# Kernel optimization log

Measured on AMD Instinct MI355X. Metric: run time of the kernel, lower is better.

## Reference

```python
import jax, jax.numpy as jnp
import numpy as np

N_NODES = 50000
N_EDGES = 1600000
IN_DIM = 128
HEADS = 4
OUT_DIM = 32
LEAKY_SLOPE = 0.2
BETA = 0.5
C = 1.2


def setup_inputs() -> dict:
    key = jax.random.key(0)
    k1, k2, k3, k4, k5, k6 = jax.random.split(key, 6)
    x = jax.random.normal(k1, (N_NODES, IN_DIM), dtype=jnp.float32)
    edge_index = jax.random.randint(k2, (2, N_EDGES), 0, N_NODES, dtype=jnp.int64)
    # GATConv params: shared linear (no bias), per-head attention vectors, output bias
    glorot = 1.0 / np.sqrt(IN_DIM)
    W = jax.random.uniform(k3, (IN_DIM, HEADS * OUT_DIM), jnp.float32, -glorot, glorot)
    att_src = jax.random.uniform(k4, (HEADS, OUT_DIM), jnp.float32, -glorot, glorot)
    att_dst = jax.random.uniform(k5, (HEADS, OUT_DIM), jnp.float32, -glorot, glorot)
    bias = jnp.zeros((HEADS * OUT_DIM,), jnp.float32)
    return {"x": x, "edge_index": edge_index, "W": W,
            "att_src": att_src, "att_dst": att_dst, "bias": bias}


def reference(x, edge_index, W, att_src, att_dst, bias):
    N = x.shape[0]
    H, D = att_src.shape
    # add self loops (edge j->i aggregates at i)
    loop = jnp.arange(N, dtype=edge_index.dtype)
    src = jnp.concatenate([edge_index[0], loop])  # [Etot]
    dst = jnp.concatenate([edge_index[1], loop])
    # per-head projection
    xp = (x @ W).reshape(N, H, D)                 # [N,H,D]
    a_src = jnp.einsum('nhd,hd->nh', xp, att_src)  # [N,H]
    a_dst = jnp.einsum('nhd,hd->nh', xp, att_dst)
    alpha = jax.nn.leaky_relu(a_src[src] + a_dst[dst], LEAKY_SLOPE)  # [Etot,H]
    # scatter-softmax over incoming edges per target node (self loops ensure coverage)
    amax = jax.ops.segment_max(alpha, dst, num_segments=N)
    e = jnp.exp(alpha - amax[dst])
    denom = jax.ops.segment_sum(e, dst, num_segments=N)
    w = e / (denom[dst] + 1e-16)                  # [Etot,H]
    # weighted scatter-add aggregation
    msg = xp[src] * w[:, :, None]                 # [Etot,H,D]
    out = jax.ops.segment_sum(msg, dst, num_segments=N).reshape(N, H * D)
    z = out + bias
    # beta-mix Swish (non-learnable swish beta = 1)
    return BETA * z + (C - BETA) * (z * jax.nn.sigmoid(z))
```

## Files before the change

### kernel.cpp

```cpp
#include <hip/hip_runtime.h>
#include <hip/hip_bf16.h>
#include <hip/hip_fp16.h>
#include <stdint.h>

#define LEAKY 0.2f
#define MIX_BETA 0.5f
#define MIX_C 1.2f

#define FBITS 6
#define FSZ   (1 << FBITS)
#define NBMX  1024
#define CH    3072
#define EPT   12
#define CAPP  2944

using short8 = __attribute__((ext_vector_type(8))) short;
using f32x4  = __attribute__((ext_vector_type(4))) float;

__device__ __forceinline__ unsigned f2bf(float f) {
    unsigned u = __float_as_uint(f);
    return (u + 0x7fffu + ((u >> 16) & 1u)) >> 16;
}
__device__ __forceinline__ unsigned pack2bf(float a, float b) {
    return f2bf(a) | (f2bf(b) << 16);
}
__device__ __forceinline__ float hlo(unsigned u) {
    return __half2float(__ushort_as_half((uint16_t)(u & 0xFFFFu)));
}
__device__ __forceinline__ float hhi(unsigned u) {
    return __half2float(__ushort_as_half((uint16_t)(u >> 16)));
}
__device__ __forceinline__ float leaky_exp(float v) {
    v = fmaxf(v, LEAKY * v);
    return __expf(v);
}

__global__ __launch_bounds__(512) void k_prep(const void* x, const void* ei, const void* W,
                                              const void* att_s, const void* att_d,
                                              const void* bias, int N, int* flags,
                                              float* att_sf, float* att_df, float* biasf,
                                              uint16_t* Wtg, int* gbcursor) {
    __shared__ uint16_t wt[128][136];
    __shared__ int lf[2];
    const int t = threadIdx.x;
    gbcursor[t] = 0; gbcursor[t + 512] = 0;
    if (t < 64) {
        const uint16_t* u = (const uint16_t*)x;
        uint16_t v = u[2 * t];
        int ef = (v >> 7) & 0xFF;
        bool ok = (ef >= 90 && ef <= 140);
        unsigned long long all_ok = __ballot(ok);
        const unsigned long long* e64 = (const unsigned long long*)ei;
        bool big = (e64[t] >= (unsigned long long)N);
        unsigned long long anybig = __ballot(big);
        if (t == 0) {
            int f0 = (all_ok == ~0ull) ? 1 : 0;
            int f1 = (anybig != 0ull) ? 1 : 0;
            flags[0] = f0; flags[1] = f1;
            lf[0] = f0; lf[1] = f1;
        }
    }
    __syncthreads();
    const bool bf = lf[0] != 0;
    if (t >= 64 && t < 448) {
        int i = t - 64;
        const void* in; float* out; int idx;
        if (i < 128)      { in = att_s; out = att_sf; idx = i; }
        else if (i < 256) { in = att_d; out = att_df; idx = i - 128; }
        else              { in = bias;  out = biasf;  idx = i - 256; }
        float v = bf ? __uint_as_float(((unsigned)((const uint16_t*)in)[idx]) << 16)
                     : ((const float*)in)[idx];
        out[idx] = v;
    }
    for (int s = t; s < 4096; s += 512) {
        int k = s >> 5, c4 = (s & 31) * 4;
        ushort4 hv;
        if (bf) {
            hv = *(const ushort4*)((const uint16_t*)W + k * 128 + c4);
        } else {
            float4 v = *(const float4*)((const float*)W + k * 128 + c4);
            hv.x = (uint16_t)f2bf(v.x); hv.y = (uint16_t)f2bf(v.y);
            hv.z = (uint16_t)f2bf(v.z); hv.w = (uint16_t)f2bf(v.w);
        }
        wt[c4 + 0][k] = hv.x; wt[c4 + 1][k] = hv.y;
        wt[c4 + 2][k] = hv.z; wt[c4 + 3][k] = hv.w;
    }
    __syncthreads();
    for (int s = t; s < 2048; s += 512) {
        int r = s >> 4, ch = (s & 15) * 8;
        *(int4*)(Wtg + r * 128 + ch) = *(const int4*)&wt[r][ch];
    }
}

__global__ __launch_bounds__(256) void k_mid(const void* x, const void* ei,
                                             const uint16_t* Wtg,
                                             const float* att_sf, const float* att_df,
                                             const int* flags, int N, int E, int G,
                                             int nb, int cap, int* gbcursor,
                                             unsigned* entries,
                                             unsigned* xph, float* a_src, float* a_dst) {
    __shared__ char smem[35840] __attribute__((aligned(16)));
    const int t = threadIdx.x;

    if ((int)blockIdx.x < G) {
        uint16_t (*xs)[136] = (uint16_t(*)[136])smem;
        const bool bf = flags[0] != 0;
        const int row0 = blockIdx.x * 128;

        for (int s = t; s < 4096; s += 256) {
            int r = s >> 5, kc = (s & 31) * 4;
            int rr = row0 + r; if (rr >= N) rr = N - 1;
            size_t g = (size_t)rr * 128 + kc;
            ushort4 hv;
            if (bf) {
                hv = *(const ushort4*)((const uint16_t*)x + g);
            } else {
                float4 v = *(const float4*)((const float*)x + g);
                hv.x = (uint16_t)f2bf(v.x); hv.y = (uint16_t)f2bf(v.y);
                hv.z = (uint16_t)f2bf(v.z); hv.w = (uint16_t)f2bf(v.w);
            }
            *(ushort4*)&xs[r][kc] = hv;
        }
        __syncthreads();

        const int w = t >> 6, l = t & 63;
        const int rA = l & 15;
        const int kg = (l >> 4) * 8;
        f32x4 acc[2][8];
#pragma unroll
        for (int fr = 0; fr < 2; ++fr)
#pragma unroll
            for (int fc = 0; fc < 8; ++fc) acc[fr][fc] = (f32x4){0.f, 0.f, 0.f, 0.f};

#pragma unroll
        for (int kk = 0; kk < 4; ++kk) {
            const int kb = kk * 32 + kg;
            short8 a0 = *(const short8*)&xs[w * 32 + rA][kb];
            short8 a1 = *(const short8*)&xs[w * 32 + 16 + rA][kb];
            const uint16_t* wp = Wtg + rA * 128 + kb;
#pragma unroll
            for (int fc = 0; fc < 8; ++fc) {
                short8 b = *(const short8*)(wp + fc * 2048);
                acc[0][fc] = __builtin_amdgcn_mfma_f32_16x16x32_bf16(a0, b, acc[0][fc], 0, 0, 0);
                acc[1][fc] = __builtin_amdgcn_mfma_f32_16x16x32_bf16(a1, b, acc[1][fc], 0, 0, 0);
            }
        }
        __syncthreads();

#pragma unroll
        for (int fr = 0; fr < 2; ++fr)
#pragma unroll
            for (int fc = 0; fc < 8; ++fc) {
                int row = w * 32 + fr * 16 + (l >> 4) * 4;
                int col = fc * 16 + rA;
#pragma unroll
                for (int j = 0; j < 4; ++j)
                    xs[row + j][col] = __half_as_ushort(__float2half(acc[fr][fc][j]));
            }
        __syncthreads();

        for (int s = t; s < 2048; s += 256) {
            int r = s >> 4, ch = (s & 15) * 8;
            int rr = row0 + r;
            if (rr < N)
                *(int4*)((uint16_t*)xph + (size_t)rr * 128 + ch) = *(const int4*)&xs[r][ch];
        }
        for (int s = t; s < 512; s += 256) {
            int r = s >> 2, hh = s & 3;
            int rr = row0 + r;
            if (rr < N) {
                float ss = 0.f, sd = 0.f;
#pragma unroll
                for (int q = 0; q < 32; ++q) {
                    float v = __half2float(__ushort_as_half(xs[r][hh * 32 + q]));
                    ss = fmaf(v, att_sf[hh * 32 + q], ss);
                    sd = fmaf(v, att_df[hh * 32 + q], sd);
                }
                a_src[(size_t)rr * 4 + hh] = ss;
                a_dst[(size_t)rr * 4 + hh] = sd;
            }
        }
    } else {
        unsigned* st  = (unsigned*)smem;
        uint16_t* bb  = (uint16_t*)(smem + 12288);
        int* lcnt     = (int*)(smem + 18432);
        int* loff     = (int*)(smem + 22528);
        int* lbase    = (int*)(smem + 26624);
        int* wcur     = (int*)(smem + 30720);
        int* sc       = (int*)(smem + 34816);
        const bool is32 = flags[1] != 0;
        const int chunk0 = ((int)blockIdx.x - G) * CH;
        const int nvalid = min(CH, E - chunk0);

        int se[EPT], de[EPT];
#pragma unroll
        for (int q = 0; q < 4; ++q) { lcnt[t + 256 * q] = 0; wcur[t + 256 * q] = 0; }
        __syncthreads();
#pragma unroll
        for (int k = 0; k < EPT; ++k) {
            int i = chunk0 + k * 256 + t;
            if (i < E) {
                int s, d;
                if (is32) { const int* p = (const int*)ei; s = p[i]; d = p[E + i]; }
                else { const long long* p = (const long long*)ei; s = (int)p[i]; d = (int)p[E + i]; }
                se[k] = s; de[k] = d;
                atomicAdd(&lcnt[d >> FBITS], 1);
            } else {
                de[k] = -1;
            }
        }
        __syncthreads();
        int c0 = lcnt[4 * t], c1 = lcnt[4 * t + 1], c2 = lcnt[4 * t + 2], c3 = lcnt[4 * t + 3];
        sc[t] = c0 + c1 + c2 + c3;
        __syncthreads();
        for (int o = 1; o < 256; o <<= 1) {
            int v = (t >= o) ? sc[t - o] : 0;
            __syncthreads();
            sc[t] += v;
            __syncthreads();
        }
        {
            int base0 = sc[t] - (c0 + c1 + c2 + c3);
            int off4[4] = {base0, base0 + c0, base0 + c0 + c1, base0 + c0 + c1 + c2};
            int cnt4[4] = {c0, c1, c2, c3};
#pragma unroll
            for (int q = 0; q < 4; ++q) {
                int k = 4 * t + q;
                loff[k] = off4[q];
                if (k < nb && cnt4[q]) {
                    int m = min(cnt4[q], cap);
                    int base = atomicAdd(&gbcursor[k], cnt4[q]);
                    if (base > cap - m) base = cap - m;
                    if (base < 0) base = 0;
                    lbase[k] = base;
                }
            }
        }
        __syncthreads();
#pragma unroll
        for (int k = 0; k < EPT; ++k) {
            int d = de[k];
            if (d >= 0) {
                int b = d >> FBITS;
                int slot = atomicAdd(&wcur[b], 1);
                int pos = loff[b] + slot;
                st[pos] = (unsigned)se[k] | ((unsigned)(d & (FSZ - 1)) << 17);
                bb[pos] = (uint16_t)b;
            }
        }
        __syncthreads();
        for (int s = t; s < nvalid; s += 256) {
            int b = bb[s];
            int pos = lbase[b] + (s - loff[b]);
            if (pos >= 0 && pos < cap)
                entries[(size_t)b * cap + pos] = st[s];
        }
    }
}

__global__ __launch_bounds__(512) void k_final(const unsigned* entries, const int* gbcursor,
                                               int cap, int N,
                                               const float* a_src, const float* a_dst,
                                               const unsigned* xph, const float* biasf,
                                               const int* flags, void* out) {
    __shared__ uint16_t ssrc_l[CAPP];
    __shared__ __half   ews_l[(CAPP / 4) * 16];
    __shared__ int ncnt[FSZ], nscan[FSZ], wcur[FSZ], poff[FSZ];
    __shared__ float adst_l[FSZ][4];
    const int b = blockIdx.x;
    const int t = threadIdx.x;
    const int node0 = b << FBITS;
    const size_t eb = (size_t)b * cap;
    const int count = min(gbcursor[b], cap);

    if (t < FSZ * 4) {
        int ln = t >> 2, hh = t & 3;
        int n = node0 + ln;
        adst_l[ln][hh] = (n < N) ? a_dst[(size_t)n * 4 + hh] : 0.f;
    }
    if (t < FSZ) ncnt[t] = 0;
    __syncthreads();
    unsigned er[6];
    int nr = 0;
    for (int i = t; i < count; i += 512) {
        unsigned e = entries[eb + i];
        er[nr++] = e;
        atomicAdd(&ncnt[e >> 17], 1);
    }
    __syncthreads();
    if (t < FSZ) nscan[t] = (ncnt[t] + 3) & ~3;
    __syncthreads();
    for (int o = 1; o < FSZ; o <<= 1) {
        int v = (t < FSZ && t >= o) ? nscan[t - o] : 0;
        __syncthreads();
        if (t < FSZ) nscan[t] += v;
        __syncthreads();
    }
    if (t < FSZ) {
        int pcnt = (ncnt[t] + 3) & ~3;
        int px = nscan[t] - pcnt;
        wcur[t] = px;
        poff[t] = px;
    }
    __syncthreads();
    if (t < FSZ) {
        int c = ncnt[t];
        int pcnt = (c + 3) & ~3;
        int px = poff[t];
        for (int p = c; p < pcnt; ++p) {
            int slot = px + p;
            ssrc_l[slot] = 0;
            __half* pe = &ews_l[(slot >> 2) * 16];
            int j = slot & 3;
            const __half z = __float2half(0.f);
            pe[j] = z; pe[4 + j] = z; pe[8 + j] = z; pe[12 + j] = z;
        }
    }
    for (int r = 0; r < nr; ++r) {
        unsigned e = er[r];
        int dlo = (int)(e >> 17);
        int s = (int)(e & 0x1FFFFu);
        int slot = atomicAdd(&wcur[dlo], 1);
        if (slot < CAPP) {
            float4 as = *(const float4*)(a_src + (size_t)s * 4);
            const float* ad = adst_l[dlo];
            float e0 = leaky_exp(as.x + ad[0]);
            float e1 = leaky_exp(as.y + ad[1]);
            float e2 = leaky_exp(as.z + ad[2]);
            float e3 = leaky_exp(as.w + ad[3]);
            ssrc_l[slot] = (uint16_t)s;
            __half* pe = &ews_l[(slot >> 2) * 16];
            int j = slot & 3;
            pe[j]      = __float2half(e0);
            pe[4 + j]  = __float2half(e1);
            pe[8 + j]  = __float2half(e2);
            pe[12 + j] = __float2half(e3);
        }
    }
    __syncthreads();

    const int wv = t >> 6, lane = t & 63;
    const int hi = lane >> 5;
    const int l = lane & 31;
    const int d0 = l * 4;
    const int h = l >> 3;
    const char* xb = (const char*)xph;
    const int outbf = flags[0];

    for (int k = wv; k < FSZ / 2; k += 8) {
        int ln = 2 * k + hi;
        int n = node0 + ln;
        bool ok = n < N;
        int nn = ok ? n : (N - 1);
        int nc = ok ? ncnt[ln] : 0;

        float adst = adst_l[ok ? ln : 0][h];
        float e = leaky_exp(a_src[(size_t)nn * 4 + h] + adst);
        uint2 xw = *(const uint2*)(xb + (size_t)nn * 256 + d0 * 2);
        float4 acc;
        acc.x = e * hlo(xw.x); acc.y = e * hhi(xw.x);
        acc.z = e * hlo(xw.y); acc.w = e * hhi(xw.y);
        float den = e;

        const int beg = ok ? poff[ln] : 0;
        const int gb = beg >> 2;
        const int ng = (nc + 3) >> 2;
        int g = 0;
        for (; g + 2 <= ng; g += 2) {
            ushort4 s4a = *(const ushort4*)&ssrc_l[beg + 4 * g];
            ushort4 s4b = *(const ushort4*)&ssrc_l[beg + 4 * g + 4];
            uint2 ea = *(const uint2*)&ews_l[(gb + g) * 16 + h * 4];
            uint2 ebw = *(const uint2*)&ews_l[(gb + g + 1) * 16 + h * 4];
            uint2 w0 = *(const uint2*)(xb + (size_t)s4a.x * 256 + d0 * 2);
            uint2 w1 = *(const uint2*)(xb + (size_t)s4a.y * 256 + d0 * 2);
            uint2 w2 = *(const uint2*)(xb + (size_t)s4a.z * 256 + d0 * 2);
            uint2 w3 = *(const uint2*)(xb + (size_t)s4a.w * 256 + d0 * 2);
            uint2 w4 = *(const uint2*)(xb + (size_t)s4b.x * 256 + d0 * 2);
            uint2 w5 = *(const uint2*)(xb + (size_t)s4b.y * 256 + d0 * 2);
            uint2 w6 = *(const uint2*)(xb + (size_t)s4b.z * 256 + d0 * 2);
            uint2 w7 = *(const uint2*)(xb + (size_t)s4b.w * 256 + d0 * 2);
            float e0 = hlo(ea.x), e1 = hhi(ea.x), e2 = hlo(ea.y), e3 = hhi(ea.y);
            float e4 = hlo(ebw.x), e5 = hhi(ebw.x), e6 = hlo(ebw.y), e7 = hhi(ebw.y);
            acc.x = fmaf(e0, hlo(w0.x), acc.x); acc.y = fmaf(e0, hhi(w0.x), acc.y);
            acc.z = fmaf(e0, hlo(w0.y), acc.z); acc.w = fmaf(e0, hhi(w0.y), acc.w);
            acc.x = fmaf(e1, hlo(w1.x), acc.x); acc.y = fmaf(e1, hhi(w1.x), acc.y);
            acc.z = fmaf(e1, hlo(w1.y), acc.z); acc.w = fmaf(e1, hhi(w1.y), acc.w);
            acc.x = fmaf(e2, hlo(w2.x), acc.x); acc.y = fmaf(e2, hhi(w2.x), acc.y);
            acc.z = fmaf(e2, hlo(w2.y), acc.z); acc.w = fmaf(e2, hhi(w2.y), acc.w);
            acc.x = fmaf(e3, hlo(w3.x), acc.x); acc.y = fmaf(e3, hhi(w3.x), acc.y);
            acc.z = fmaf(e3, hlo(w3.y), acc.z); acc.w = fmaf(e3, hhi(w3.y), acc.w);
            acc.x = fmaf(e4, hlo(w4.x), acc.x); acc.y = fmaf(e4, hhi(w4.x), acc.y);
            acc.z = fmaf(e4, hlo(w4.y), acc.z); acc.w = fmaf(e4, hhi(w4.y), acc.w);
            acc.x = fmaf(e5, hlo(w5.x), acc.x); acc.y = fmaf(e5, hhi(w5.x), acc.y);
            acc.z = fmaf(e5, hlo(w5.y), acc.z); acc.w = fmaf(e5, hhi(w5.y), acc.w);
            acc.x = fmaf(e6, hlo(w6.x), acc.x); acc.y = fmaf(e6, hhi(w6.x), acc.y);
            acc.z = fmaf(e6, hlo(w6.y), acc.z); acc.w = fmaf(e6, hhi(w6.y), acc.w);
            acc.x = fmaf(e7, hlo(w7.x), acc.x); acc.y = fmaf(e7, hhi(w7.x), acc.y);
            acc.z = fmaf(e7, hlo(w7.y), acc.z); acc.w = fmaf(e7, hhi(w7.y), acc.w);
            den += ((e0 + e1) + (e2 + e3)) + ((e4 + e5) + (e6 + e7));
        }
        if (g < ng) {
            ushort4 s4 = *(const ushort4*)&ssrc_l[beg + 4 * g];
            uint2 ea = *(const uint2*)&ews_l[(gb + g) * 16 + h * 4];
            float e0 = hlo(ea.x), e1 = hhi(ea.x), e2 = hlo(ea.y), e3 = hhi(ea.y);
            uint2 w0 = *(const uint2*)(xb + (size_t)s4.x * 256 + d0 * 2);
            uint2 w1 = *(const uint2*)(xb + (size_t)s4.y * 256 + d0 * 2);
            uint2 w2 = *(const uint2*)(xb + (size_t)s4.z * 256 + d0 * 2);
            uint2 w3 = *(const uint2*)(xb + (size_t)s4.w * 256 + d0 * 2);
            acc.x = fmaf(e0, hlo(w0.x), acc.x); acc.y = fmaf(e0, hhi(w0.x), acc.y);
            acc.z = fmaf(e0, hlo(w0.y), acc.z); acc.w = fmaf(e0, hhi(w0.y), acc.w);
            acc.x = fmaf(e1, hlo(w1.x), acc.x); acc.y = fmaf(e1, hhi(w1.x), acc.y);
            acc.z = fmaf(e1, hlo(w1.y), acc.z); acc.w = fmaf(e1, hhi(w1.y), acc.w);
            acc.x = fmaf(e2, hlo(w2.x), acc.x); acc.y = fmaf(e2, hhi(w2.x), acc.y);
            acc.z = fmaf(e2, hlo(w2.y), acc.z); acc.w = fmaf(e2, hhi(w2.y), acc.w);
            acc.x = fmaf(e3, hlo(w3.x), acc.x); acc.y = fmaf(e3, hhi(w3.x), acc.y);
            acc.z = fmaf(e3, hlo(w3.y), acc.z); acc.w = fmaf(e3, hhi(w3.y), acc.w);
            den += (e0 + e1) + (e2 + e3);
        }
        float inv = 1.f / (den + 1e-16f);
        float4 bv = *(const float4*)(biasf + d0);
        float z0 = fmaf(acc.x, inv, bv.x);
        float z1 = fmaf(acc.y, inv, bv.y);
        float z2 = fmaf(acc.z, inv, bv.z);
        float z3 = fmaf(acc.w, inv, bv.w);
        float r0 = MIX_BETA * z0 + (MIX_C - MIX_BETA) * z0 / (1.f + __expf(-z0));
        float r1 = MIX_BETA * z1 + (MIX_C - MIX_BETA) * z1 / (1.f + __expf(-z1));
        float r2 = MIX_BETA * z2 + (MIX_C - MIX_BETA) * z2 / (1.f + __expf(-z2));
        float r3 = MIX_BETA * z3 + (MIX_C - MIX_BETA) * z3 / (1.f + __expf(-z3));
        if (ok) {
            if (outbf) {
                uint2 ov = make_uint2(pack2bf(r0, r1), pack2bf(r2, r3));
                *(uint2*)((uint16_t*)out + (size_t)n * 128 + d0) = ov;
            } else {
                *(float4*)((float*)out + (size_t)n * 128 + d0) = make_float4(r0, r1, r2, r3);
            }
        }
    }
}

extern "C" void kernel_launch(void* const* d_in, const int* in_sizes, int n_in,
                              void* d_out, int out_size, void* d_ws, size_t ws_size,
                              hipStream_t stream) {
    const void* x     = d_in[0];
    const void* ei    = d_in[1];
    const void* W     = d_in[2];
    const void* att_s = d_in[3];
    const void* att_d = d_in[4];
    const void* bias  = d_in[5];
    const int N = in_sizes[0] / 128;
    const int E = in_sizes[1] / 2;
    const int NB = (N + FSZ - 1) >> FBITS;
    int cap = E / NB + E / (8 * NB) + 256;
    const int capmax = CAPP - 3 * FSZ - 8;
    if (cap > capmax) cap = capmax;

    char* ws = (char*)d_ws;
    size_t off = 0;
    auto alloc = [&](size_t bytes) -> void* {
        void* p = ws + off;
        off += (bytes + 255) & ~(size_t)255;
        return p;
    };
    int* flags        = (int*)alloc(16);
    unsigned* entries = (unsigned*)alloc((size_t)NB * cap * 4);
    int* gbcursor     = (int*)alloc(NBMX * 4);
    unsigned* xph     = (unsigned*)alloc((size_t)N * 64 * 4);
    float* a_src      = (float*)alloc((size_t)N * 4 * 4);
    float* a_dst      = (float*)alloc((size_t)N * 4 * 4);
    float* att_sf     = (float*)alloc(128 * 4);
    float* att_df     = (float*)alloc(128 * 4);
    float* biasf      = (float*)alloc(128 * 4);
    uint16_t* Wtg     = (uint16_t*)alloc(128 * 128 * 2);

    const int G = (N + 127) / 128;
    const int S = (E + CH - 1) / CH;

    k_prep<<<1, 512, 0, stream>>>(x, ei, W, att_s, att_d, bias, N, flags,
                                  att_sf, att_df, biasf, Wtg, gbcursor);
    k_mid<<<G + S, 256, 0, stream>>>(x, ei, Wtg, att_sf, att_df, flags, N, E, G,
                                     NB, cap, gbcursor, entries, xph, a_src, a_dst);
    k_final<<<NB, 512, 0, stream>>>(entries, gbcursor, cap, N, a_src, a_dst,
                                    xph, biasf, flags, d_out);
}
```

Measured before the change: 138.1 us.

## Double destination bucket size and widen per-lane gathers to 8 features

Destination buckets grow from 64 to 128 nodes, so there are fewer buckets, the binning chunks are larger and the final kernel runs with 1024 threads per block. In the aggregation loop each lane now loads 16-byte feature slices (8 halves) instead of 8 bytes, with 16 lanes covering a node and 4 nodes per wave. The goal is fewer, wider gather transactions and fewer global atomics on bucket cursors. The cost is much larger shared memory per final block and a larger capacity margin, which may lower occupancy and leave fewer blocks than CUs.

```diff
diff --git a/kernel.cpp b/kernel.cpp
--- a/kernel.cpp
+++ b/kernel.cpp
@@ -7,12 +7,12 @@
 #define MIX_BETA 0.5f
 #define MIX_C 1.2f
 
-#define FBITS 6
+#define FBITS 7
 #define FSZ   (1 << FBITS)
-#define NBMX  1024
-#define CH    3072
-#define EPT   12
-#define CAPP  2944
+#define NBMX  512
+#define CH    4096
+#define EPT   16
+#define CAPP  5632
 
 using short8 = __attribute__((ext_vector_type(8))) short;
 using f32x4  = __attribute__((ext_vector_type(4))) float;
@@ -33,6 +33,12 @@
 __device__ __forceinline__ float leaky_exp(float v) {
     v = fmaxf(v, LEAKY * v);
     return __expf(v);
+}
+__device__ __forceinline__ void fma8(float* acc, float e, uint4 w) {
+    acc[0] = fmaf(e, hlo(w.x), acc[0]); acc[1] = fmaf(e, hhi(w.x), acc[1]);
+    acc[2] = fmaf(e, hlo(w.y), acc[2]); acc[3] = fmaf(e, hhi(w.y), acc[3]);
+    acc[4] = fmaf(e, hlo(w.z), acc[4]); acc[5] = fmaf(e, hhi(w.z), acc[5]);
+    acc[6] = fmaf(e, hlo(w.w), acc[6]); acc[7] = fmaf(e, hhi(w.w), acc[7]);
 }
 
 __global__ __launch_bounds__(512) void k_prep(const void* x, const void* ei, const void* W,
@@ -43,7 +49,7 @@
     __shared__ uint16_t wt[128][136];
     __shared__ int lf[2];
     const int t = threadIdx.x;
-    gbcursor[t] = 0; gbcursor[t + 512] = 0;
+    if (t < NBMX) gbcursor[t] = 0;
     if (t < 64) {
         const uint16_t* u = (const uint16_t*)x;
         uint16_t v = u[2 * t];
@@ -99,7 +105,7 @@
                                              int nb, int cap, int* gbcursor,
                                              unsigned* entries,
                                              unsigned* xph, float* a_src, float* a_dst) {
-    __shared__ char smem[35840] __attribute__((aligned(16)));
+    __shared__ char smem[40960] __attribute__((aligned(16)));
     const int t = threadIdx.x;
 
     if ((int)blockIdx.x < G) {
@@ -182,19 +188,19 @@
         }
     } else {
         unsigned* st  = (unsigned*)smem;
-        uint16_t* bb  = (uint16_t*)(smem + 12288);
-        int* lcnt     = (int*)(smem + 18432);
-        int* loff     = (int*)(smem + 22528);
-        int* lbase    = (int*)(smem + 26624);
+        uint16_t* bb  = (uint16_t*)(smem + 16384);
+        int* lcnt     = (int*)(smem + 24576);
+        int* loff     = (int*)(smem + 26624);
+        int* lbase    = (int*)(smem + 28672);
         int* wcur     = (int*)(smem + 30720);
-        int* sc       = (int*)(smem + 34816);
+        int* sc       = (int*)(smem + 32768);
         const bool is32 = flags[1] != 0;
         const int chunk0 = ((int)blockIdx.x - G) * CH;
         const int nvalid = min(CH, E - chunk0);
 
         int se[EPT], de[EPT];
-#pragma unroll
-        for (int q = 0; q < 4; ++q) { lcnt[t + 256 * q] = 0; wcur[t + 256 * q] = 0; }
+        lcnt[t] = 0; lcnt[t + 256] = 0;
+        wcur[t] = 0; wcur[t + 256] = 0;
         __syncthreads();
 #pragma unroll
         for (int k = 0; k < EPT; ++k) {
@@ -210,8 +216,8 @@
             }
         }
         __syncthreads();
-        int c0 = lcnt[4 * t], c1 = lcnt[4 * t + 1], c2 = lcnt[4 * t + 2], c3 = lcnt[4 * t + 3];
-        sc[t] = c0 + c1 + c2 + c3;
+        int c0 = lcnt[2 * t], c1 = lcnt[2 * t + 1];
+        sc[t] = c0 + c1;
         __syncthreads();
         for (int o = 1; o < 256; o <<= 1) {
             int v = (t >= o) ? sc[t - o] : 0;
@@ -220,16 +226,17 @@
             __syncthreads();
         }
         {
-            int base0 = sc[t] - (c0 + c1 + c2 + c3);
-            int off4[4] = {base0, base0 + c0, base0 + c0 + c1, base0 + c0 + c1 + c2};
-            int cnt4[4] = {c0, c1, c2, c3};
-#pragma unroll
-            for (int q = 0; q < 4; ++q) {
-                int k = 4 * t + q;
-                loff[k] = off4[q];
-                if (k < nb && cnt4[q]) {
-                    int m = min(cnt4[q], cap);
-                    int base = atomicAdd(&gbcursor[k], cnt4[q]);
+            int excl = sc[t] - (c0 + c1);
+            int k0 = 2 * t, k1 = 2 * t + 1;
+            loff[k0] = excl;
+            loff[k1] = excl + c0;
+            int cnt2[2] = {c0, c1};
+#pragma unroll
+            for (int q = 0; q < 2; ++q) {
+                int k = k0 + q;
+                if (k < nb && cnt2[q]) {
+                    int m = min(cnt2[q], cap);
+                    int base = atomicAdd(&gbcursor[k], cnt2[q]);
                     if (base > cap - m) base = cap - m;
                     if (base < 0) base = 0;
                     lbase[k] = base;
@@ -258,11 +265,11 @@
     }
 }
 
-__global__ __launch_bounds__(512) void k_final(const unsigned* entries, const int* gbcursor,
-                                               int cap, int N,
-                                               const float* a_src, const float* a_dst,
-                                               const unsigned* xph, const float* biasf,
-                                               const int* flags, void* out) {
+__global__ __launch_bounds__(1024) void k_final(const unsigned* entries, const int* gbcursor,
+                                                int cap, int N,
+                                                const float* a_src, const float* a_dst,
+                                                const unsigned* xph, const float* biasf,
+                                                const int* flags, void* out) {
     __shared__ uint16_t ssrc_l[CAPP];
     __shared__ __half   ews_l[(CAPP / 4) * 16];
     __shared__ int ncnt[FSZ], nscan[FSZ], wcur[FSZ], poff[FSZ];
@@ -282,7 +289,7 @@
     __syncthreads();
     unsigned er[6];
     int nr = 0;
-    for (int i = t; i < count; i += 512) {
+    for (int i = t; i < count; i += 1024) {
         unsigned e = entries[eb + i];
         er[nr++] = e;
         atomicAdd(&ncnt[e >> 17], 1);
@@ -307,17 +314,17 @@
         int c = ncnt[t];
         int pcnt = (c + 3) & ~3;
         int px = poff[t];
+        const __half z = __float2half(0.f);
         for (int p = c; p < pcnt; ++p) {
             int slot = px + p;
             ssrc_l[slot] = 0;
             __half* pe = &ews_l[(slot >> 2) * 16];
             int j = slot & 3;
-            const __half z = __float2half(0.f);
             pe[j] = z; pe[4 + j] = z; pe[8 + j] = z; pe[12 + j] = z;
         }
     }
-    for (int r = 0; r < nr; ++r) {
-        unsigned e = er[r];
+    for (int r2 = 0; r2 < nr; ++r2) {
+        unsigned e = er[r2];
         int dlo = (int)(e >> 17);
         int s = (int)(e & 0x1FFFFu);
         int slot = atomicAdd(&wcur[dlo], 1);
@@ -340,15 +347,15 @@
     __syncthreads();
 
     const int wv = t >> 6, lane = t & 63;
-    const int hi = lane >> 5;
-    const int l = lane & 31;
-    const int d0 = l * 4;
-    const int h = l >> 3;
+    const int hi = lane >> 4;
+    const int l = lane & 15;
+    const int d0 = l * 8;
+    const int h = l >> 2;
     const char* xb = (const char*)xph;
     const int outbf = flags[0];
 
-    for (int k = wv; k < FSZ / 2; k += 8) {
-        int ln = 2 * k + hi;
+    for (int k = wv; k < FSZ / 4; k += 16) {
+        int ln = 4 * k + hi;
         int n = node0 + ln;
         bool ok = n < N;
         int nn = ok ? n : (N - 1);
@@ -356,10 +363,12 @@
 
         float adst = adst_l[ok ? ln : 0][h];
         float e = leaky_exp(a_src[(size_t)nn * 4 + h] + adst);
-        uint2 xw = *(const uint2*)(xb + (size_t)nn * 256 + d0 * 2);
-        float4 acc;
-        acc.x = e * hlo(xw.x); acc.y = e * hhi(xw.x);
-        acc.z = e * hlo(xw.y); acc.w = e * hhi(xw.y);
+        uint4 xw = *(const uint4*)(xb + (size_t)nn * 256 + d0 * 2);
+        float acc[8];
+        acc[0] = e * hlo(xw.x); acc[1] = e * hhi(xw.x);
+        acc[2] = e * hlo(xw.y); acc[3] = e * hhi(xw.y);
+        acc[4] = e * hlo(xw.z); acc[5] = e * hhi(xw.z);
+        acc[6] = e * hlo(xw.w); acc[7] = e * hhi(xw.w);
         float den = e;
 
         const int beg = ok ? poff[ln] : 0;
@@ -369,70 +378,58 @@
         for (; g + 2 <= ng; g += 2) {
             ushort4 s4a = *(const ushort4*)&ssrc_l[beg + 4 * g];
             ushort4 s4b = *(const ushort4*)&ssrc_l[beg + 4 * g + 4];
-            uint2 ea = *(const uint2*)&ews_l[(gb + g) * 16 + h * 4];
-            uint2 ebw = *(const uint2*)&ews_l[(gb + g + 1) * 16 + h * 4];
-            uint2 w0 = *(const uint2*)(xb + (size_t)s4a.x * 256 + d0 * 2);
-            uint2 w1 = *(const uint2*)(xb + (size_t)s4a.y * 256 + d0 * 2);
-            uint2 w2 = *(const uint2*)(xb + (size_t)s4a.z * 256 + d0 * 2);
-            uint2 w3 = *(const uint2*)(xb + (size_t)s4a.w * 256 + d0 * 2);
-            uint2 w4 = *(const uint2*)(xb + (size_t)s4b.x * 256 + d0 * 2);
-            uint2 w5 = *(const uint2*)(xb + (size_t)s4b.y * 256 + d0 * 2);
-            uint2 w6 = *(const uint2*)(xb + (size_t)s4b.z * 256 + d0 * 2);
-            uint2 w7 = *(const uint2*)(xb + (size_t)s4b.w * 256 + d0 * 2);
+            uint2 ea  = *(const uint2*)&ews_l[(gb + g) * 16 + h * 4];
+            uint2 eb2 = *(const uint2*)&ews_l[(gb + g + 1) * 16 + h * 4];
+            uint4 w0 = *(const uint4*)(xb + (size_t)s4a.x * 256 + d0 * 2);
+            uint4 w1 = *(const uint4*)(xb + (size_t)s4a.y * 256 + d0 * 2);
+            uint4 w2 = *(const uint4*)(xb + (size_t)s4a.z * 256 + d0 * 2);
+            uint4 w3 = *(const uint4*)(xb + (size_t)s4a.w * 256 + d0 * 2);
+            uint4 w4 = *(const uint4*)(xb + (size_t)s4b.x * 256 + d0 * 2);
+            uint4 w5 = *(const uint4*)(xb + (size_t)s4b.y * 256 + d0 * 2);
+            uint4 w6 = *(const uint4*)(xb + (size_t)s4b.z * 256 + d0 * 2);
+            uint4 w7 = *(const uint4*)(xb + (size_t)s4b.w * 256 + d0 * 2);
             float e0 = hlo(ea.x), e1 = hhi(ea.x), e2 = hlo(ea.y), e3 = hhi(ea.y);
-            float e4 = hlo(ebw.x), e5 = hhi(ebw.x), e6 = hlo(ebw.y), e7 = hhi(ebw.y);
-            acc.x = fmaf(e0, hlo(w0.x), acc.x); acc.y = fmaf(e0, hhi(w0.x), acc.y);
-            acc.z = fmaf(e0, hlo(w0.y), acc.z); acc.w = fmaf(e0, hhi(w0.y), acc.w);
-            acc.x = fmaf(e1, hlo(w1.x), acc.x); acc.y = fmaf(e1, hhi(w1.x), acc.y);
-            acc.z = fmaf(e1, hlo(w1.y), acc.z); acc.w = fmaf(e1, hhi(w1.y), acc.w);
-            acc.x = fmaf(e2, hlo(w2.x), acc.x); acc.y = fmaf(e2, hhi(w2.x), acc.y);
-            acc.z = fmaf(e2, hlo(w2.y), acc.z); acc.w = fmaf(e2, hhi(w2.y), acc.w);
-            acc.x = fmaf(e3, hlo(w3.x), acc.x); acc.y = fmaf(e3, hhi(w3.x), acc.y);
-            acc.z = fmaf(e3, hlo(w3.y), acc.z); acc.w = fmaf(e3, hhi(w3.y), acc.w);
-            acc.x = fmaf(e4, hlo(w4.x), acc.x); acc.y = fmaf(e4, hhi(w4.x), acc.y);
-            acc.z = fmaf(e4, hlo(w4.y), acc.z); acc.w = fmaf(e4, hhi(w4.y), acc.w);
-            acc.x = fmaf(e5, hlo(w5.x), acc.x); acc.y = fmaf(e5, hhi(w5.x), acc.y);
-            acc.z = fmaf(e5, hlo(w5.y), acc.z); acc.w = fmaf(e5, hhi(w5.y), acc.w);
-            acc.x = fmaf(e6, hlo(w6.x), acc.x); acc.y = fmaf(e6, hhi(w6.x), acc.y);
-            acc.z = fmaf(e6, hlo(w6.y), acc.z); acc.w = fmaf(e6, hhi(w6.y), acc.w);
-            acc.x = fmaf(e7, hlo(w7.x), acc.x); acc.y = fmaf(e7, hhi(w7.x), acc.y);
-            acc.z = fmaf(e7, hlo(w7.y), acc.z); acc.w = fmaf(e7, hhi(w7.y), acc.w);
+            float e4 = hlo(eb2.x), e5 = hhi(eb2.x), e6 = hlo(eb2.y), e7 = hhi(eb2.y);
+            fma8(acc, e0, w0); fma8(acc, e1, w1);
+            fma8(acc, e2, w2); fma8(acc, e3, w3);
+            fma8(acc, e4, w4); fma8(acc, e5, w5);
+            fma8(acc, e6, w6); fma8(acc, e7, w7);
             den += ((e0 + e1) + (e2 + e3)) + ((e4 + e5) + (e6 + e7));
         }
         if (g < ng) {
             ushort4 s4 = *(const ushort4*)&ssrc_l[beg + 4 * g];
             uint2 ea = *(const uint2*)&ews_l[(gb + g) * 16 + h * 4];
             float e0 = hlo(ea.x), e1 = hhi(ea.x), e2 = hlo(ea.y), e3 = hhi(ea.y);
-            uint2 w0 = *(const uint2*)(xb + (size_t)s4.x * 256 + d0 * 2);
-            uint2 w1 = *(const uint2*)(xb + (size_t)s4.y * 256 + d0 * 2);
-            uint2 w2 = *(const uint2*)(xb + (size_t)s4.z * 256 + d0 * 2);
-            uint2 w3 = *(const uint2*)(xb + (size_t)s4.w * 256 + d0 * 2);
-            acc.x = fmaf(e0, hlo(w0.x), acc.x); acc.y = fmaf(e0, hhi(w0.x), acc.y);
-            acc.z = fmaf(e0, hlo(w0.y), acc.z); acc.w = fmaf(e0, hhi(w0.y), acc.w);
-            acc.x = fmaf(e1, hlo(w1.x), acc.x); acc.y = fmaf(e1, hhi(w1.x), acc.y);
-            acc.z = fmaf(e1, hlo(w1.y), acc.z); acc.w = fmaf(e1, hhi(w1.y), acc.w);
-            acc.x = fmaf(e2, hlo(w2.x), acc.x); acc.y = fmaf(e2, hhi(w2.x), acc.y);
-            acc.z = fmaf(e2, hlo(w2.y), acc.z); acc.w = fmaf(e2, hhi(w2.y), acc.w);
-            acc.x = fmaf(e3, hlo(w3.x), acc.x); acc.y = fmaf(e3, hhi(w3.x), acc.y);
-            acc.z = fmaf(e3, hlo(w3.y), acc.z); acc.w = fmaf(e3, hhi(w3.y), acc.w);
+            uint4 w0 = *(const uint4*)(xb + (size_t)s4.x * 256 + d0 * 2);
+            uint4 w1 = *(const uint4*)(xb + (size_t)s4.y * 256 + d0 * 2);
+            uint4 w2 = *(const uint4*)(xb + (size_t)s4.z * 256 + d0 * 2);
+            uint4 w3 = *(const uint4*)(xb + (size_t)s4.w * 256 + d0 * 2);
+            fma8(acc, e0, w0); fma8(acc, e1, w1);
+            fma8(acc, e2, w2); fma8(acc, e3, w3);
             den += (e0 + e1) + (e2 + e3);
         }
         float inv = 1.f / (den + 1e-16f);
-        float4 bv = *(const float4*)(biasf + d0);
-        float z0 = fmaf(acc.x, inv, bv.x);
-        float z1 = fmaf(acc.y, inv, bv.y);
-        float z2 = fmaf(acc.z, inv, bv.z);
-        float z3 = fmaf(acc.w, inv, bv.w);
-        float r0 = MIX_BETA * z0 + (MIX_C - MIX_BETA) * z0 / (1.f + __expf(-z0));
-        float r1 = MIX_BETA * z1 + (MIX_C - MIX_BETA) * z1 / (1.f + __expf(-z1));
-        float r2 = MIX_BETA * z2 + (MIX_C - MIX_BETA) * z2 / (1.f + __expf(-z2));
-        float r3 = MIX_BETA * z3 + (MIX_C - MIX_BETA) * z3 / (1.f + __expf(-z3));
+        float4 bv0 = *(const float4*)(biasf + d0);
+        float4 bv1 = *(const float4*)(biasf + d0 + 4);
+        float z[8];
+        z[0] = fmaf(acc[0], inv, bv0.x); z[1] = fmaf(acc[1], inv, bv0.y);
+        z[2] = fmaf(acc[2], inv, bv0.z); z[3] = fmaf(acc[3], inv, bv0.w);
+        z[4] = fmaf(acc[4], inv, bv1.x); z[5] = fmaf(acc[5], inv, bv1.y);
+        z[6] = fmaf(acc[6], inv, bv1.z); z[7] = fmaf(acc[7], inv, bv1.w);
+        float r[8];
+#pragma unroll
+        for (int j = 0; j < 8; ++j)
+            r[j] = MIX_BETA * z[j] + (MIX_C - MIX_BETA) * z[j] / (1.f + __expf(-z[j]));
         if (ok) {
             if (outbf) {
-                uint2 ov = make_uint2(pack2bf(r0, r1), pack2bf(r2, r3));
-                *(uint2*)((uint16_t*)out + (size_t)n * 128 + d0) = ov;
+                uint4 ov;
+                ov.x = pack2bf(r[0], r[1]); ov.y = pack2bf(r[2], r[3]);
+                ov.z = pack2bf(r[4], r[5]); ov.w = pack2bf(r[6], r[7]);
+                *(uint4*)((uint16_t*)out + (size_t)n * 128 + d0) = ov;
             } else {
-                *(float4*)((float*)out + (size_t)n * 128 + d0) = make_float4(r0, r1, r2, r3);
+                float* po = (float*)out + (size_t)n * 128 + d0;
+                *(float4*)po       = make_float4(r[0], r[1], r[2], r[3]);
+                *(float4*)(po + 4) = make_float4(r[4], r[5], r[6], r[7]);
             }
         }
     }
@@ -450,7 +447,7 @@
     const int N = in_sizes[0] / 128;
     const int E = in_sizes[1] / 2;
     const int NB = (N + FSZ - 1) >> FBITS;
-    int cap = E / NB + E / (8 * NB) + 256;
+    int cap = E / NB + E / (8 * NB) + 512;
     const int capmax = CAPP - 3 * FSZ - 8;
     if (cap > capmax) cap = capmax;
 
@@ -479,6 +476,6 @@
                                   att_sf, att_df, biasf, Wtg, gbcursor);
     k_mid<<<G + S, 256, 0, stream>>>(x, ei, Wtg, att_sf, att_df, flags, N, E, G,
                                      NB, cap, gbcursor, entries, xph, a_src, a_dst);
-    k_final<<<NB, 512, 0, stream>>>(entries, gbcursor, cap, N, a_src, a_dst,
-                                    xph, biasf, flags, d_out);
-}
+    k_final<<<NB, 1024, 0, stream>>>(entries, gbcursor, cap, N, a_src, a_dst,
+                                     xph, biasf, flags, d_out);
+}
```

Measured after the change: 114.6 us. 1.21x faster.
